# Kernel tuning notes

Measured on AMD Instinct MI355X. Metric: run time of the kernel, lower is better.

Reference implementation:

```python
import jax, jax.numpy as jnp
import numpy as np
from jax import lax

B, N, C, RED = 8, 2048, 1024, 4
GN_EPS = 1e-5


def setup_inputs() -> dict:
    key = jax.random.key(0)
    ks = jax.random.split(key, 8)
    s = lambda k, shp, sc: jax.random.normal(k, shp, jnp.float32) * sc
    return dict(
        x=jax.random.normal(ks[0], (B, N, C), jnp.float32),
        qkv_w=s(ks[1], (C, 3 * C), 0.02),
        c1=jnp.float32(0.01 ** 2),
        c2=jnp.float32(0.03 ** 2),
        conv1_w=s(ks[2], (4, 1, 3), 0.3),      # OIH
        gn_g=jnp.ones(4, jnp.float32),
        gn_b=jnp.zeros(4, jnp.float32),
        conv2_w=s(ks[3], (1, 4, 3), 0.3),      # OIH
        conv2_b=jnp.zeros(1, jnp.float32),
        ch_w1=s(ks[4], (C, C // RED), 0.02),
        ch_b1=jnp.zeros(C // RED, jnp.float32),
        ch_w2=s(ks[5], (C // RED, C), 0.02),
        ch_b2=jnp.zeros(C, jnp.float32),
        proj_w=s(ks[6], (C, C), 0.02),
        proj_b=jnp.zeros(C, jnp.float32),
    )


def _conv1d(x, w):  # x:[B,Cin,N], w:[O,I,3], pad=1
    return lax.conv_general_dilated(x, w, (1,), [(1, 1)],
                                    dimension_numbers=('NCH', 'OIH', 'NCH'))


def _ode_func(A, conv1_w, gn_g, gn_b, conv2_w, conv2_b):
    # A: [B,N] -> Conv1d(1,4) -> GroupNorm(2,4) -> ReLU -> Conv1d(4,1)
    h = _conv1d(A[:, None, :], conv1_w)                 # [B,4,N]
    b, _, n = h.shape
    hg = h.reshape(b, 2, 2, n)                          # 2 groups of 2 channels
    mu = hg.mean((2, 3), keepdims=True)
    var = hg.var((2, 3), keepdims=True)
    h = ((hg - mu) * lax.rsqrt(var + GN_EPS)).reshape(b, 4, n)
    h = jax.nn.relu(h * gn_g[None, :, None] + gn_b[None, :, None])
    y = _conv1d(h, conv2_w) + conv2_b[None, :, None]    # [B,1,N]
    return y[:, 0, :]


def reference(x, qkv_w, c1, c2, conv1_w, gn_g, gn_b, conv2_w, conv2_b,
              ch_w1, ch_b1, ch_w2, ch_b2, proj_w, proj_b):
    Bx, Nx, Cx = x.shape
    qkv = (x @ qkv_w).reshape(Bx, Nx, 3, Cx)
    q, k, v = qkv[..., 0, :], qkv[..., 1, :], qkv[..., 2, :]

    # SSIM-style per-token statistics over the channel dim
    mu_q = q.mean(-1, keepdims=True)
    mu_k = k.mean(-1, keepdims=True)
    dq, dk = q - mu_q, k - mu_k
    inv_cm1 = 1.0 / (Cx - 1)
    sigma_qk = (dq * dk).sum(-1, keepdims=True) * inv_cm1
    sigma_q2 = (dq * dq).sum(-1, keepdims=True) * inv_cm1
    sigma_k2 = (dk * dk).sum(-1, keepdims=True) * inv_cm1
    num = (2 * mu_q * mu_k + c1) * (2 * sigma_qk + c2)
    den = (mu_q ** 2 + mu_k ** 2 + c1) * (sigma_q2 + sigma_k2 + c2)
    attn_base = ((num / (den + 1e-7)) ** 2)[..., 0]     # [B,N]

    # explicit-Euler integration over t = linspace(0,1,2) -> one step, dt=1
    steps = 2
    ts = jnp.linspace(0.0, 1.0, steps)
    dts = ts[1:] - ts[:-1]

    def step(A, dt):
        return A + dt * _ode_func(A, conv1_w, gn_g, gn_b, conv2_w, conv2_b), None

    A, _ = lax.scan(step, attn_base, dts)
    final_a = jax.nn.sigmoid(A)                         # [B,N]
    weights = jax.nn.softmax(final_a, axis=1)           # softmax over tokens

    # channel gating from mean token
    m = x.mean(axis=1, keepdims=True)                   # [B,1,C]
    ch_w = jax.nn.sigmoid(jax.nn.relu(m @ ch_w1 + ch_b1) @ ch_w2 + ch_b2)

    out_low = weights[..., None] * v * ch_w             # [B,N,C]
    return out_low @ proj_w + proj_b
```

## Files before the change

kernel.cpp:

```cpp
#include <hip/hip_runtime.h>

typedef __attribute__((ext_vector_type(8))) short short8;
typedef __attribute__((ext_vector_type(4))) short short4v;
typedef __attribute__((ext_vector_type(4))) float floatx4;

__device__ __forceinline__ unsigned short f2bf(float f) {
    unsigned u = __float_as_uint(f);
    u = u + 0x7fffu + ((u >> 16) & 1u);
    return (unsigned short)(u >> 16);
}

__device__ __forceinline__ void gl_lds16(const void* g, void* l) {
    __builtin_amdgcn_global_load_lds((const __attribute__((address_space(1))) void*)g,
                                     (__attribute__((address_space(3))) void*)l, 16, 0, 0);
}

__global__ __launch_bounds__(256) void convmean_kernel(const float* __restrict__ x,
                                                       short* __restrict__ xb,
                                                       float* __restrict__ part) {
    int bid = blockIdx.x;
    int b = bid >> 6, nch = bid & 63;
    int tid = threadIdx.x;
    size_t base = ((size_t)b * 2048 + nch * 32) * 1024;
    float s0 = 0.f, s1 = 0.f, s2 = 0.f, s3 = 0.f;
    int c0 = tid * 4;
    for (int r = 0; r < 32; r++) {
        const float* rp = x + base + (size_t)r * 1024 + c0;
        float4 v = *(const float4*)rp;
        s0 += v.x; s1 += v.y; s2 += v.z; s3 += v.w;
        short4v o;
        o[0] = (short)f2bf(v.x); o[1] = (short)f2bf(v.y);
        o[2] = (short)f2bf(v.z); o[3] = (short)f2bf(v.w);
        *(short4v*)(xb + base + (size_t)r * 1024 + c0) = o;
    }
    float* pp = part + ((size_t)b * 64 + nch) * 1024 + c0;
    float4 ps; ps.x = s0; ps.y = s1; ps.z = s2; ps.w = s3;
    *(float4*)pp = ps;
}

__global__ __launch_bounds__(256) void transpose_conv_kernel(const float* __restrict__ w_qkv,
                                                             short* __restrict__ qkvT,
                                                             const float* __restrict__ w_proj,
                                                             short* __restrict__ projT) {
    __shared__ float t[64][65];
    int bx = blockIdx.x;
    const float* in; short* out; int C; bool is_qkv;
    int c0, r0 = blockIdx.y * 64;
    if (bx < 48) { in = w_qkv; out = qkvT; C = 3072; c0 = bx * 64; is_qkv = true; }
    else         { in = w_proj; out = projT; C = 1024; c0 = (bx - 48) * 64; is_qkv = false; }
    int tid = threadIdx.x;
#pragma unroll
    for (int l = 0; l < 16; l++) {
        int idx = l * 256 + tid;
        int rr = idx >> 6, cc = idx & 63;
        t[rr][cc] = in[(size_t)(r0 + rr) * C + c0 + cc];
    }
    __syncthreads();
#pragma unroll
    for (int l = 0; l < 16; l++) {
        int idx = l * 256 + tid;
        int rr = idx >> 6, cc = idx & 63;
        int ro = c0 + rr;
        int rnew = ro;
        if (is_qkv) {
            if (ro < 1024) rnew = 2 * ro;
            else if (ro < 2048) rnew = 2 * (ro - 1024) + 1;
        }
        out[(size_t)rnew * 1024 + r0 + cc] = (short)f2bf(t[cc][rr]);
    }
}

__global__ __launch_bounds__(256) void ch_kernel(const float* __restrict__ part,
                                                 const float* __restrict__ w1,
                                                 const float* __restrict__ b1,
                                                 const float* __restrict__ w2,
                                                 const float* __restrict__ b2,
                                                 float* __restrict__ ch) {
    int b = blockIdx.x >> 3, cg = blockIdx.x & 7;
    int tid = threadIdx.x;
    __shared__ float mrow[1024];
    __shared__ float hid[256];
    for (int i = tid; i < 1024; i += 256) {
        float s = 0.f;
        for (int j = 0; j < 64; j++) s += part[((size_t)b * 64 + j) * 1024 + i];
        mrow[i] = s * (1.f / 2048.f);
    }
    __syncthreads();
    {
        float s0 = 0.f, s1 = 0.f, s2 = 0.f, s3 = 0.f;
        for (int i = 0; i < 1024; i += 4) {
            s0 += mrow[i] * w1[(size_t)i * 256 + tid];
            s1 += mrow[i + 1] * w1[(size_t)(i + 1) * 256 + tid];
            s2 += mrow[i + 2] * w1[(size_t)(i + 2) * 256 + tid];
            s3 += mrow[i + 3] * w1[(size_t)(i + 3) * 256 + tid];
        }
        hid[tid] = fmaxf((s0 + s1) + (s2 + s3) + b1[tid], 0.f);
    }
    __syncthreads();
    if (tid < 128) {
        int c = cg * 128 + tid;
        float s0 = 0.f, s1 = 0.f, s2 = 0.f, s3 = 0.f;
        for (int j = 0; j < 256; j += 4) {
            s0 += hid[j] * w2[(size_t)j * 1024 + c];
            s1 += hid[j + 1] * w2[(size_t)(j + 1) * 1024 + c];
            s2 += hid[j + 2] * w2[(size_t)(j + 2) * 1024 + c];
            s3 += hid[j + 3] * w2[(size_t)(j + 3) * 1024 + c];
        }
        float s = (s0 + s1) + (s2 + s3) + b2[c];
        ch[(size_t)b * 1024 + c] = 1.f / (1.f + expf(-s));
    }
}


#define QKV_PHASE(qq)                                                                   \
    {                                                                                   \
        _Pragma("unroll")                                                               \
        for (int ii = 0; ii < 4; ii++)                                                  \
            af[ii] = *(const short8*)(As_ + (wm * 128 + ((qq)*4 + ii) * 16 + ar) * 32 + swq); \
        __builtin_amdgcn_s_setprio(1);                                                  \
        _Pragma("unroll")                                                               \
        for (int ii = 0; ii < 4; ii++)                                                  \
            _Pragma("unroll")                                                           \
            for (int jj = 0; jj < 4; jj++)                                              \
                acc[(qq)*4 + ii][jj] =                                                  \
                    __builtin_amdgcn_mfma_f32_16x16x32_bf16(af[ii], bfr[jj], acc[(qq)*4 + ii][jj], 0, 0, 0); \
        __builtin_amdgcn_s_setprio(0);                                                  \
    }

#define LOAD_B()                                                                        \
    {                                                                                   \
        _Pragma("unroll")                                                               \
        for (int jj = 0; jj < 4; jj++)                                                  \
            bfr[jj] = *(const short8*)(Bs_ + (wn * 64 + jj * 16 + ar) * 32 + swq);      \
    }

__global__ __launch_bounds__(512, 2) void gemm_qkv_kernel(const short* __restrict__ A,
                                                          const short* __restrict__ BT,
                                                          short* __restrict__ vbuf,
                                                          const float* __restrict__ ch,
                                                          float* __restrict__ part2)
{
    __shared__ __align__(16) short ASf[4 * 8192];
    __shared__ __align__(16) short BSf[4 * 8192];
    const int tid = threadIdx.x;
    const int wave = tid >> 6, lane = tid & 63;
    const int id = blockIdx.x;
    const int xcd = id & 7, j = id >> 3;
    const int bn = j % 12;
    const int bmg = j / 12;
    const int bm = bmg * 8 + xcd;
    const int wm = wave >> 2, wn = wave & 3;
    const int ar = lane & 15, quad = lane >> 4;
    const int swq = (quad ^ ((ar >> 1) & 3)) * 8;

    const int swzk = ((lane & 3) ^ ((lane >> 3) & 3)) * 8;
    const short* Ag = A + (size_t)(bm * 256 + wave * 32 + (lane >> 2)) * 1024 + swzk;
    const short* Bg = BT + (size_t)(bn * 256 + wave * 32 + (lane >> 2)) * 1024 + swzk;
    short* ASw = ASf + wave * 1024;
    short* BSw = BSf + wave * 1024;

    floatx4 acc[8][4];
    floatx4 zero = {0.f, 0.f, 0.f, 0.f};
#pragma unroll
    for (int i = 0; i < 8; i++)
#pragma unroll
        for (int jj = 0; jj < 4; jj++) acc[i][jj] = zero;

    auto stageA = [&](int t) {
        const int sl = (t & 3) * 8192, ko = t * 32;
        gl_lds16(Ag + ko, ASw + sl);
        gl_lds16(Ag + (size_t)16 * 1024 + ko, ASw + sl + 512);
    };
    auto stageB = [&](int t) {
        const int sl = (t & 3) * 8192, ko = t * 32;
        gl_lds16(Bg + ko, BSw + sl);
        gl_lds16(Bg + (size_t)16 * 1024 + ko, BSw + sl + 512);
    };

    short8 af[4], bfr[4];

    stageA(0); stageB(0); stageA(1); stageB(1);
    for (int t = 0; t < 30; ++t) {
        stageA(t + 2);
        asm volatile("s_waitcnt vmcnt(6)" ::: "memory");
        asm volatile("s_barrier" ::: "memory");
        const short* As_ = ASf + (t & 3) * 8192;
        const short* Bs_ = BSf + (t & 3) * 8192;
        LOAD_B();
        QKV_PHASE(0);
        stageB(t + 2);
        QKV_PHASE(1);
    }
    {
        asm volatile("s_waitcnt vmcnt(4)" ::: "memory");
        asm volatile("s_barrier" ::: "memory");
        const short* As_ = ASf + (30 & 3) * 8192;
        const short* Bs_ = BSf + (30 & 3) * 8192;
        LOAD_B();
        QKV_PHASE(0);
        QKV_PHASE(1);
    }
    {
        asm volatile("s_waitcnt vmcnt(0)" ::: "memory");
        asm volatile("s_barrier" ::: "memory");
        const short* As_ = ASf + (31 & 3) * 8192;
        const short* Bs_ = BSf + (31 & 3) * 8192;
        LOAD_B();
        QKV_PHASE(0);
        QKV_PHASE(1);
    }
    __syncthreads();

    if (bn < 8) {
        float* sb = (float*)ASf;
#pragma unroll
        for (int i = 0; i < 8; i++) {
            float st[4][5];
#pragma unroll
            for (int r = 0; r < 4; r++)
#pragma unroll
                for (int f = 0; f < 5; f++) st[r][f] = 0.f;
#pragma unroll
            for (int jj = 0; jj < 4; jj++) {
#pragma unroll
                for (int r = 0; r < 4; r++) {
                    float val = acc[i][jj][r];
                    float other = __shfl_xor(val, 1);
                    float q = (lane & 1) ? other : val;
                    float kv = (lane & 1) ? val : other;
                    st[r][0] += q; st[r][1] += kv;
                    st[r][2] += q * q; st[r][3] += kv * kv; st[r][4] += q * kv;
                }
            }
#pragma unroll
            for (int r = 0; r < 4; r++)
#pragma unroll
                for (int f = 0; f < 5; f++) {
                    float v = st[r][f];
                    v += __shfl_xor(v, 2);
                    v += __shfl_xor(v, 4);
                    v += __shfl_xor(v, 8);
                    st[r][f] = v;
                }
            if ((lane & 15) == 0) {
#pragma unroll
                for (int r = 0; r < 4; r++)
#pragma unroll
                    for (int f = 0; f < 5; f++)
                        sb[(size_t)(wn * 256 + wm * 128 + i * 16 + quad * 4 + r) * 5 + f] = st[r][f];
            }
        }
        __syncthreads();
        if (tid < 256) {
#pragma unroll
            for (int f = 0; f < 5; f++) {
                float s = sb[(size_t)(0 * 256 + tid) * 5 + f] + sb[(size_t)(1 * 256 + tid) * 5 + f] +
                          sb[(size_t)(2 * 256 + tid) * 5 + f] + sb[(size_t)(3 * 256 + tid) * 5 + f];
                part2[(size_t)(bn * 5 + f) * 16384 + bm * 256 + tid] = s;
            }
        }
    } else {
        const int batch = bm >> 3;
        const int vcol0 = bn * 256 - 2048 + wn * 64;
        short* pbuf = (short*)ASf + wave * 1024;
        float cw[4];
#pragma unroll
        for (int jj = 0; jj < 4; jj++) cw[jj] = ch[(size_t)batch * 1024 + vcol0 + jj * 16 + ar];
#pragma unroll
        for (int i = 0; i < 8; i++) {
#pragma unroll
            for (int jj = 0; jj < 4; jj++)
#pragma unroll
                for (int r = 0; r < 4; r++)
                    pbuf[(quad * 4 + r) * 64 + jj * 16 + ar] = (short)f2bf(acc[i][jj][r] * cw[jj]);
#pragma unroll
            for (int p = 0; p < 2; p++) {
                int idx = p * 512 + lane * 8;
                short8 vv = *(const short8*)(pbuf + idx);
                int grow = bm * 256 + wm * 128 + i * 16 + (idx >> 6);
                int gcol = vcol0 + (idx & 63);
                *(short8*)(vbuf + (size_t)grow * 1024 + gcol) = vv;
            }
        }
    }
}

__global__ __launch_bounds__(256) void finalize_kernel(const float* __restrict__ part2,
                                                       const float* __restrict__ c1p,
                                                       const float* __restrict__ c2p,
                                                       float* __restrict__ attn) {
    int row = blockIdx.x * 256 + threadIdx.x;
    float s[5] = {0.f, 0.f, 0.f, 0.f, 0.f};
#pragma unroll
    for (int slot = 0; slot < 8; slot++)
#pragma unroll
        for (int f = 0; f < 5; f++)
            s[f] += part2[(size_t)((slot * 5 + f) << 14) + row];
    const float C = 1024.f, invcm1 = 1.f / 1023.f;
    float c1 = *c1p, c2 = *c2p;
    float muq = s[0] / C, muk = s[1] / C;
    float sigqk = (s[4] - C * muq * muk) * invcm1;
    float sigq2 = (s[2] - C * muq * muq) * invcm1;
    float sigk2 = (s[3] - C * muk * muk) * invcm1;
    float num = (2.f * muq * muk + c1) * (2.f * sigqk + c2);
    float den = (muq * muq + muk * muk + c1) * (sigq2 + sigk2 + c2);
    float r = num / (den + 1e-7f);
    attn[row] = r * r;
}

__device__ __forceinline__ float blk_sum(float v, float* buf) {
#pragma unroll
    for (int m = 1; m < 64; m <<= 1) v += __shfl_xor(v, m);
    int wave = threadIdx.x >> 6;
    if ((threadIdx.x & 63) == 0) buf[wave] = v;
    __syncthreads();
    float r = buf[0] + buf[1] + buf[2] + buf[3];
    __syncthreads();
    return r;
}
__device__ __forceinline__ float blk_max(float v, float* buf) {
#pragma unroll
    for (int m = 1; m < 64; m <<= 1) v = fmaxf(v, __shfl_xor(v, m));
    int wave = threadIdx.x >> 6;
    if ((threadIdx.x & 63) == 0) buf[wave] = v;
    __syncthreads();
    float r = fmaxf(fmaxf(buf[0], buf[1]), fmaxf(buf[2], buf[3]));
    __syncthreads();
    return r;
}

__global__ __launch_bounds__(256) void ode_softmax_kernel(const float* __restrict__ attn,
                                                          const float* __restrict__ w1,
                                                          const float* __restrict__ gng,
                                                          const float* __restrict__ gnb,
                                                          const float* __restrict__ w2,
                                                          const float* __restrict__ b2,
                                                          float* __restrict__ wgt) {
    int b = blockIdx.x, tid = threadIdx.x;
    __shared__ float A0[2048];
    __shared__ float H[4][2048];
    __shared__ float rbuf[4];
    for (int i = tid; i < 2048; i += 256) A0[i] = attn[(size_t)b * 2048 + i];
    __syncthreads();
    float w1l[12], w2l[12];
#pragma unroll
    for (int i = 0; i < 12; i++) { w1l[i] = w1[i]; w2l[i] = w2[i]; }
    float gg[4], gb[4];
#pragma unroll
    for (int c = 0; c < 4; c++) { gg[c] = gng[c]; gb[c] = gnb[c]; }

    float s0 = 0.f, ss0 = 0.f, s1 = 0.f, ss1 = 0.f;
    for (int i = tid; i < 2048; i += 256) {
        float le = (i > 0) ? A0[i - 1] : 0.f;
        float mi = A0[i];
        float ri = (i < 2047) ? A0[i + 1] : 0.f;
#pragma unroll
        for (int c = 0; c < 4; c++) {
            float h = w1l[c * 3] * le + w1l[c * 3 + 1] * mi + w1l[c * 3 + 2] * ri;
            H[c][i] = h;
            if (c < 2) { s0 += h; ss0 += h * h; } else { s1 += h; ss1 += h * h; }
        }
    }
    s0 = blk_sum(s0, rbuf);
    ss0 = blk_sum(ss0, rbuf);
    s1 = blk_sum(s1, rbuf);
    ss1 = blk_sum(ss1, rbuf);
    float mu0 = s0 / 4096.f, var0 = ss0 / 4096.f - mu0 * mu0;
    float mu1 = s1 / 4096.f, var1 = ss1 / 4096.f - mu1 * mu1;
    float is0 = 1.f / sqrtf(var0 + 1e-5f);
    float is1 = 1.f / sqrtf(var1 + 1e-5f);

    for (int i = tid; i < 2048; i += 256) {
#pragma unroll
        for (int c = 0; c < 4; c++) {
            float inv = (c < 2) ? is0 : is1;
            float mu = (c < 2) ? mu0 : mu1;
            float v = (H[c][i] - mu) * inv * gg[c] + gb[c];
            H[c][i] = fmaxf(v, 0.f);
        }
    }
    __syncthreads();

    float bias2 = b2[0];
    float myfa[8];
    float lmax = -1e30f;
#pragma unroll
    for (int ii = 0; ii < 8; ii++) {
        int i = tid + ii * 256;
        float y = bias2;
#pragma unroll
        for (int c = 0; c < 4; c++) {
            float le = (i > 0) ? H[c][i - 1] : 0.f;
            float mi = H[c][i];
            float ri = (i < 2047) ? H[c][i + 1] : 0.f;
            y += w2l[c * 3] * le + w2l[c * 3 + 1] * mi + w2l[c * 3 + 2] * ri;
        }
        float Av = A0[i] + y;
        float fa = 1.f / (1.f + expf(-Av));
        myfa[ii] = fa;
        lmax = fmaxf(lmax, fa);
    }
    float gmax = blk_max(lmax, rbuf);
    float lsum = 0.f;
#pragma unroll
    for (int ii = 0; ii < 8; ii++) {
        myfa[ii] = expf(myfa[ii] - gmax);
        lsum += myfa[ii];
    }
    float gsum = blk_sum(lsum, rbuf);
    float inv = 1.f / gsum;
#pragma unroll
    for (int ii = 0; ii < 8; ii++) wgt[(size_t)b * 2048 + tid + ii * 256] = myfa[ii] * inv;
}

__global__ __launch_bounds__(512, 2) void gemm_out_kernel(const short* __restrict__ vbuf,
                                                          const short* __restrict__ BT,
                                                          const float* __restrict__ wgt,
                                                          const float* __restrict__ pb,
                                                          float* __restrict__ Out)
{
    __shared__ __align__(16) short ASf[4 * 8192];
    __shared__ __align__(16) short BSf[4 * 8192];
    const int tid = threadIdx.x;
    const int wave = tid >> 6, lane = tid & 63;
    const int id = blockIdx.x;
    const int xcd = id & 7, j = id >> 3;
    const int bn = j & 3;
    const int bmg = j >> 2;
    const int bm = bmg * 8 + xcd;
    const int wm = wave >> 2, wn = wave & 3;
    const int ar = lane & 15, quad = lane >> 4;
    const int swq = (quad ^ ((ar >> 1) & 3)) * 8;

    const int swzk = ((lane & 3) ^ ((lane >> 3) & 3)) * 8;
    const short* Ag = vbuf + (size_t)(bm * 256 + wave * 32 + (lane >> 2)) * 1024 + swzk;
    const short* Bg = BT + (size_t)(bn * 256 + wave * 32 + (lane >> 2)) * 1024 + swzk;
    short* ASw = ASf + wave * 1024;
    short* BSw = BSf + wave * 1024;

    floatx4 acc[8][4];
    floatx4 zero = {0.f, 0.f, 0.f, 0.f};
#pragma unroll
    for (int i = 0; i < 8; i++)
#pragma unroll
        for (int jj = 0; jj < 4; jj++) acc[i][jj] = zero;

    auto stageA = [&](int t) {
        const int sl = (t & 3) * 8192, ko = t * 32;
        gl_lds16(Ag + ko, ASw + sl);
        gl_lds16(Ag + (size_t)16 * 1024 + ko, ASw + sl + 512);
    };
    auto stageB = [&](int t) {
        const int sl = (t & 3) * 8192, ko = t * 32;
        gl_lds16(Bg + ko, BSw + sl);
        gl_lds16(Bg + (size_t)16 * 1024 + ko, BSw + sl + 512);
    };

    short8 af[4], bfr[4];

    stageA(0); stageB(0); stageA(1); stageB(1);
    for (int t = 0; t < 30; ++t) {
        stageA(t + 2);
        asm volatile("s_waitcnt vmcnt(6)" ::: "memory");
        asm volatile("s_barrier" ::: "memory");
        const short* As_ = ASf + (t & 3) * 8192;
        const short* Bs_ = BSf + (t & 3) * 8192;
        LOAD_B();
        QKV_PHASE(0);
        stageB(t + 2);
        QKV_PHASE(1);
    }
    {
        asm volatile("s_waitcnt vmcnt(4)" ::: "memory");
        asm volatile("s_barrier" ::: "memory");
        const short* As_ = ASf + (30 & 3) * 8192;
        const short* Bs_ = BSf + (30 & 3) * 8192;
        LOAD_B();
        QKV_PHASE(0);
        QKV_PHASE(1);
    }
    {
        asm volatile("s_waitcnt vmcnt(0)" ::: "memory");
        asm volatile("s_barrier" ::: "memory");
        const short* As_ = ASf + (31 & 3) * 8192;
        const short* Bs_ = BSf + (31 & 3) * 8192;
        LOAD_B();
        QKV_PHASE(0);
        QKV_PHASE(1);
    }
    __syncthreads();

    const int row0 = bm * 256 + wm * 128;
    const int col0 = bn * 256 + wn * 64;
    float* obuf = (float*)ASf + wave * 1024;
#pragma unroll
    for (int i = 0; i < 8; i++) {
#pragma unroll
        for (int jj = 0; jj < 4; jj++) {
            float bias = pb[col0 + jj * 16 + ar];
#pragma unroll
            for (int r = 0; r < 4; r++) {
                int grow = row0 + i * 16 + quad * 4 + r;
                obuf[(quad * 4 + r) * 64 + jj * 16 + ar] = wgt[grow] * acc[i][jj][r] + bias;
            }
        }
#pragma unroll
        for (int p = 0; p < 4; p++) {
            int idx = p * 256 + lane * 4;
            float4 vv = *(const float4*)(obuf + idx);
            int grow = row0 + i * 16 + (idx >> 6);
            int gcol = col0 + (idx & 63);
            *(float4*)(Out + (size_t)grow * 1024 + gcol) = vv;
        }
    }
}

extern "C" void kernel_launch(void* const* d_in, const int* in_sizes, int n_in,
                              void* d_out, int out_size, void* d_ws, size_t ws_size,
                              hipStream_t stream) {
    const float* x       = (const float*)d_in[0];
    const float* qkv_w   = (const float*)d_in[1];
    const float* c1      = (const float*)d_in[2];
    const float* c2      = (const float*)d_in[3];
    const float* conv1_w = (const float*)d_in[4];
    const float* gn_g    = (const float*)d_in[5];
    const float* gn_b    = (const float*)d_in[6];
    const float* conv2_w = (const float*)d_in[7];
    const float* conv2_b = (const float*)d_in[8];
    const float* ch_w1   = (const float*)d_in[9];
    const float* ch_b1   = (const float*)d_in[10];
    const float* ch_w2   = (const float*)d_in[11];
    const float* ch_b2   = (const float*)d_in[12];
    const float* proj_w  = (const float*)d_in[13];
    const float* proj_b  = (const float*)d_in[14];
    float* out = (float*)d_out;

    size_t off = 0;
    char* base = (char*)d_ws;
    auto carve = [&](size_t bytes) -> char* {
        char* p = base + off;
        off += (bytes + 255) & ~(size_t)255;
        return p;
    };
    short* x_bf  = (short*)carve((size_t)16384 * 1024 * 2);
    short* qkvT  = (short*)carve((size_t)3072 * 1024 * 2);
    short* projT = (short*)carve((size_t)1024 * 1024 * 2);
    short* vbuf  = (short*)carve((size_t)16384 * 1024 * 2);
    float* part2 = (float*)carve((size_t)80 * 16384 * 4);
    float* attn  = (float*)carve((size_t)16384 * 4);
    float* wgt   = (float*)carve((size_t)16384 * 4);
    float* part  = (float*)carve((size_t)8 * 64 * 1024 * 4);
    float* chw   = (float*)carve((size_t)8 * 1024 * 4);

    convmean_kernel<<<512, 256, 0, stream>>>(x, x_bf, part);
    transpose_conv_kernel<<<dim3(64, 16), 256, 0, stream>>>(qkv_w, qkvT, proj_w, projT);
    ch_kernel<<<64, 256, 0, stream>>>(part, ch_w1, ch_b1, ch_w2, ch_b2, chw);
    gemm_qkv_kernel<<<768, 512, 0, stream>>>(x_bf, qkvT, vbuf, chw, part2);
    finalize_kernel<<<64, 256, 0, stream>>>(part2, c1, c2, attn);
    ode_softmax_kernel<<<8, 256, 0, stream>>>(attn, conv1_w, gn_g, gn_b, conv2_w, conv2_b, wgt);
    gemm_out_kernel<<<256, 512, 0, stream>>>(vbuf, projT, wgt, proj_b, out);
}
```

Baseline: 390.9 us.

## Restructure GEMM main loop into ping-pong LDS-fragment and MFMA phases with extra barriers

Both bf16 GEMM kernels now load LDS fragments into two separate A-fragment register sets and issue global-to-LDS staging between the fragment reads and the MFMA blocks. Barriers are placed inside each half-iteration, and the vmcnt wait moves to the end of the iteration. The aim is to overlap LDS reads and global prefetch with MFMA work and keep waves in lockstep in a ping-pong style schedule. The cost is more barriers per iteration and more register pressure from the second A-fragment array, which could hurt occupancy at launch bounds 512,2.

```diff
diff --git a/kernel.cpp b/kernel.cpp
--- a/kernel.cpp
+++ b/kernel.cpp
@@ -112,26 +112,30 @@
 }
 
 
-#define QKV_PHASE(qq)                                                                   \
+#define LOAD_BF()                                                                       \
+    {                                                                                   \
+        _Pragma("unroll")                                                               \
+        for (int jj = 0; jj < 4; jj++)                                                  \
+            bfr[jj] = *(const short8*)(Bs_ + (wn * 64 + jj * 16 + ar) * 32 + swq);      \
+    }
+
+#define LOAD_AF(dst, qq)                                                                \
     {                                                                                   \
         _Pragma("unroll")                                                               \
         for (int ii = 0; ii < 4; ii++)                                                  \
-            af[ii] = *(const short8*)(As_ + (wm * 128 + ((qq)*4 + ii) * 16 + ar) * 32 + swq); \
+            dst[ii] = *(const short8*)(As_ + (wm * 128 + ((qq)*4 + ii) * 16 + ar) * 32 + swq); \
+    }
+
+#define MFMA_Q(afv, qq)                                                                 \
+    {                                                                                   \
         __builtin_amdgcn_s_setprio(1);                                                  \
         _Pragma("unroll")                                                               \
         for (int ii = 0; ii < 4; ii++)                                                  \
             _Pragma("unroll")                                                           \
             for (int jj = 0; jj < 4; jj++)                                              \
                 acc[(qq)*4 + ii][jj] =                                                  \
-                    __builtin_amdgcn_mfma_f32_16x16x32_bf16(af[ii], bfr[jj], acc[(qq)*4 + ii][jj], 0, 0, 0); \
+                    __builtin_amdgcn_mfma_f32_16x16x32_bf16(afv[ii], bfr[jj], acc[(qq)*4 + ii][jj], 0, 0, 0); \
         __builtin_amdgcn_s_setprio(0);                                                  \
-    }
-
-#define LOAD_B()                                                                        \
-    {                                                                                   \
-        _Pragma("unroll")                                                               \
-        for (int jj = 0; jj < 4; jj++)                                                  \
-            bfr[jj] = *(const short8*)(Bs_ + (wn * 64 + jj * 16 + ar) * 32 + swq);      \
     }
 
 __global__ __launch_bounds__(512, 2) void gemm_qkv_kernel(const short* __restrict__ A,
@@ -177,37 +181,40 @@
         gl_lds16(Bg + (size_t)16 * 1024 + ko, BSw + sl + 512);
     };
 
-    short8 af[4], bfr[4];
+    short8 af0[4], af1[4], bfr[4];
 
     stageA(0); stageB(0); stageA(1); stageB(1);
+    asm volatile("s_waitcnt vmcnt(4)" ::: "memory");
+    asm volatile("s_barrier" ::: "memory");
     for (int t = 0; t < 30; ++t) {
-        stageA(t + 2);
-        asm volatile("s_waitcnt vmcnt(6)" ::: "memory");
-        asm volatile("s_barrier" ::: "memory");
         const short* As_ = ASf + (t & 3) * 8192;
         const short* Bs_ = BSf + (t & 3) * 8192;
-        LOAD_B();
-        QKV_PHASE(0);
+        LOAD_BF();
+        LOAD_AF(af0, 0);
+        stageA(t + 2);
+        asm volatile("s_barrier" ::: "memory");
+        MFMA_Q(af0, 0);
+        LOAD_AF(af1, 1);
         stageB(t + 2);
-        QKV_PHASE(1);
-    }
-    {
+        asm volatile("s_barrier" ::: "memory");
+        MFMA_Q(af1, 1);
         asm volatile("s_waitcnt vmcnt(4)" ::: "memory");
         asm volatile("s_barrier" ::: "memory");
-        const short* As_ = ASf + (30 & 3) * 8192;
-        const short* Bs_ = BSf + (30 & 3) * 8192;
-        LOAD_B();
-        QKV_PHASE(0);
-        QKV_PHASE(1);
-    }
-    {
-        asm volatile("s_waitcnt vmcnt(0)" ::: "memory");
-        asm volatile("s_barrier" ::: "memory");
-        const short* As_ = ASf + (31 & 3) * 8192;
-        const short* Bs_ = BSf + (31 & 3) * 8192;
-        LOAD_B();
-        QKV_PHASE(0);
-        QKV_PHASE(1);
+    }
+    for (int t = 30; t < 32; ++t) {
+        const short* As_ = ASf + (t & 3) * 8192;
+        const short* Bs_ = BSf + (t & 3) * 8192;
+        LOAD_BF();
+        LOAD_AF(af0, 0);
+        asm volatile("s_barrier" ::: "memory");
+        MFMA_Q(af0, 0);
+        LOAD_AF(af1, 1);
+        asm volatile("s_barrier" ::: "memory");
+        MFMA_Q(af1, 1);
+        if (t == 30) {
+            asm volatile("s_waitcnt vmcnt(0)" ::: "memory");
+            asm volatile("s_barrier" ::: "memory");
+        }
     }
     __syncthreads();
 
@@ -456,37 +463,40 @@
         gl_lds16(Bg + (size_t)16 * 1024 + ko, BSw + sl + 512);
     };
 
-    short8 af[4], bfr[4];
+    short8 af0[4], af1[4], bfr[4];
 
     stageA(0); stageB(0); stageA(1); stageB(1);
+    asm volatile("s_waitcnt vmcnt(4)" ::: "memory");
+    asm volatile("s_barrier" ::: "memory");
     for (int t = 0; t < 30; ++t) {
-        stageA(t + 2);
-        asm volatile("s_waitcnt vmcnt(6)" ::: "memory");
-        asm volatile("s_barrier" ::: "memory");
         const short* As_ = ASf + (t & 3) * 8192;
         const short* Bs_ = BSf + (t & 3) * 8192;
-        LOAD_B();
-        QKV_PHASE(0);
+        LOAD_BF();
+        LOAD_AF(af0, 0);
+        stageA(t + 2);
+        asm volatile("s_barrier" ::: "memory");
+        MFMA_Q(af0, 0);
+        LOAD_AF(af1, 1);
         stageB(t + 2);
-        QKV_PHASE(1);
-    }
-    {
+        asm volatile("s_barrier" ::: "memory");
+        MFMA_Q(af1, 1);
         asm volatile("s_waitcnt vmcnt(4)" ::: "memory");
         asm volatile("s_barrier" ::: "memory");
-        const short* As_ = ASf + (30 & 3) * 8192;
-        const short* Bs_ = BSf + (30 & 3) * 8192;
-        LOAD_B();
-        QKV_PHASE(0);
-        QKV_PHASE(1);
-    }
-    {
-        asm volatile("s_waitcnt vmcnt(0)" ::: "memory");
-        asm volatile("s_barrier" ::: "memory");
-        const short* As_ = ASf + (31 & 3) * 8192;
-        const short* Bs_ = BSf + (31 & 3) * 8192;
-        LOAD_B();
-        QKV_PHASE(0);
-        QKV_PHASE(1);
+    }
+    for (int t = 30; t < 32; ++t) {
+        const short* As_ = ASf + (t & 3) * 8192;
+        const short* Bs_ = BSf + (t & 3) * 8192;
+        LOAD_BF();
+        LOAD_AF(af0, 0);
+        asm volatile("s_barrier" ::: "memory");
+        MFMA_Q(af0, 0);
+        LOAD_AF(af1, 1);
+        asm volatile("s_barrier" ::: "memory");
+        MFMA_Q(af1, 1);
+        if (t == 30) {
+            asm volatile("s_waitcnt vmcnt(0)" ::: "memory");
+            asm volatile("s_barrier" ::: "memory");
+        }
     }
     __syncthreads();
 
```

Result: slower. 399.7 us (+2.3%).

## Interleave GEMM main loop into four barrier-separated phases with split staging loads

Applied to the files above, without the earlier changes.

Restructures the K-loop of both bf16 GEMM kernels so each tile is processed in four phases of two A-fragment rows, each issuing one global-to-LDS load and then a workgroup barrier before its MFMAs. The aim is to spread memory issue evenly across the MFMA stream and keep the waves in lockstep, ping-pong style, so LDS reads and global loads overlap compute better. It adds several extra barriers per tile, which can cost throughput if the waves drift apart. It also moves the waitcnt to the end of each tile.

```diff
diff --git a/kernel.cpp b/kernel.cpp
--- a/kernel.cpp
+++ b/kernel.cpp
@@ -112,26 +112,44 @@
 }
 
 
-#define QKV_PHASE(qq)                                                                   \
-    {                                                                                   \
-        _Pragma("unroll")                                                               \
-        for (int ii = 0; ii < 4; ii++)                                                  \
-            af[ii] = *(const short8*)(As_ + (wm * 128 + ((qq)*4 + ii) * 16 + ar) * 32 + swq); \
-        __builtin_amdgcn_s_setprio(1);                                                  \
-        _Pragma("unroll")                                                               \
-        for (int ii = 0; ii < 4; ii++)                                                  \
-            _Pragma("unroll")                                                           \
-            for (int jj = 0; jj < 4; jj++)                                              \
-                acc[(qq)*4 + ii][jj] =                                                  \
-                    __builtin_amdgcn_mfma_f32_16x16x32_bf16(af[ii], bfr[jj], acc[(qq)*4 + ii][jj], 0, 0, 0); \
-        __builtin_amdgcn_s_setprio(0);                                                  \
-    }
-
-#define LOAD_B()                                                                        \
+#define LDB4()                                                                          \
     {                                                                                   \
         _Pragma("unroll")                                                               \
         for (int jj = 0; jj < 4; jj++)                                                  \
             bfr[jj] = *(const short8*)(Bs_ + (wn * 64 + jj * 16 + ar) * 32 + swq);      \
+    }
+
+#define PH(qq, STAGE)                                                                   \
+    {                                                                                   \
+        short8 a0 = *(const short8*)(As_ + (wm * 128 + ((qq)*2 + 0) * 16 + ar) * 32 + swq); \
+        short8 a1 = *(const short8*)(As_ + (wm * 128 + ((qq)*2 + 1) * 16 + ar) * 32 + swq); \
+        STAGE;                                                                          \
+        asm volatile("s_barrier" ::: "memory");                                         \
+        __builtin_amdgcn_sched_barrier(0);                                              \
+        __builtin_amdgcn_s_setprio(1);                                                  \
+        _Pragma("unroll")                                                               \
+        for (int jj = 0; jj < 4; jj++)                                                  \
+            acc[(qq)*2 + 0][jj] =                                                       \
+                __builtin_amdgcn_mfma_f32_16x16x32_bf16(a0, bfr[jj], acc[(qq)*2 + 0][jj], 0, 0, 0); \
+        _Pragma("unroll")                                                               \
+        for (int jj = 0; jj < 4; jj++)                                                  \
+            acc[(qq)*2 + 1][jj] =                                                       \
+                __builtin_amdgcn_mfma_f32_16x16x32_bf16(a1, bfr[jj], acc[(qq)*2 + 1][jj], 0, 0, 0); \
+        __builtin_amdgcn_s_setprio(0);                                                  \
+    }
+
+#define TILE_BODY(T, SA0, SA1, SB0, SB1)                                                \
+    {                                                                                   \
+        const short* As_ = ASf + ((T) & 3) * 8192;                                      \
+        const short* Bs_ = BSf + ((T) & 3) * 8192;                                      \
+        LDB4();                                                                         \
+        PH(0, SA0);                                                                     \
+        asm volatile("s_barrier" ::: "memory");                                         \
+        PH(1, SA1);                                                                     \
+        asm volatile("s_barrier" ::: "memory");                                         \
+        PH(2, SB0);                                                                     \
+        asm volatile("s_barrier" ::: "memory");                                         \
+        PH(3, SB1);                                                                     \
     }
 
 __global__ __launch_bounds__(512, 2) void gemm_qkv_kernel(const short* __restrict__ A,
@@ -166,49 +184,26 @@
 #pragma unroll
         for (int jj = 0; jj < 4; jj++) acc[i][jj] = zero;
 
-    auto stageA = [&](int t) {
-        const int sl = (t & 3) * 8192, ko = t * 32;
-        gl_lds16(Ag + ko, ASw + sl);
-        gl_lds16(Ag + (size_t)16 * 1024 + ko, ASw + sl + 512);
-    };
-    auto stageB = [&](int t) {
-        const int sl = (t & 3) * 8192, ko = t * 32;
-        gl_lds16(Bg + ko, BSw + sl);
-        gl_lds16(Bg + (size_t)16 * 1024 + ko, BSw + sl + 512);
-    };
-
-    short8 af[4], bfr[4];
-
-    stageA(0); stageB(0); stageA(1); stageB(1);
+    auto stA0 = [&](int t) { gl_lds16(Ag + t * 32, ASw + (t & 3) * 8192); };
+    auto stA1 = [&](int t) { gl_lds16(Ag + (size_t)16 * 1024 + t * 32, ASw + (t & 3) * 8192 + 512); };
+    auto stB0 = [&](int t) { gl_lds16(Bg + t * 32, BSw + (t & 3) * 8192); };
+    auto stB1 = [&](int t) { gl_lds16(Bg + (size_t)16 * 1024 + t * 32, BSw + (t & 3) * 8192 + 512); };
+
+    short8 bfr[4];
+
+    stA0(0); stA1(0); stB0(0); stB1(0);
+    stA0(1); stA1(1); stB0(1); stB1(1);
+    asm volatile("s_waitcnt vmcnt(4)" ::: "memory");
+    asm volatile("s_barrier" ::: "memory");
     for (int t = 0; t < 30; ++t) {
-        stageA(t + 2);
-        asm volatile("s_waitcnt vmcnt(6)" ::: "memory");
-        asm volatile("s_barrier" ::: "memory");
-        const short* As_ = ASf + (t & 3) * 8192;
-        const short* Bs_ = BSf + (t & 3) * 8192;
-        LOAD_B();
-        QKV_PHASE(0);
-        stageB(t + 2);
-        QKV_PHASE(1);
-    }
-    {
+        TILE_BODY(t, stA0(t + 2), stA1(t + 2), stB0(t + 2), stB1(t + 2));
         asm volatile("s_waitcnt vmcnt(4)" ::: "memory");
         asm volatile("s_barrier" ::: "memory");
-        const short* As_ = ASf + (30 & 3) * 8192;
-        const short* Bs_ = BSf + (30 & 3) * 8192;
-        LOAD_B();
-        QKV_PHASE(0);
-        QKV_PHASE(1);
-    }
-    {
-        asm volatile("s_waitcnt vmcnt(0)" ::: "memory");
-        asm volatile("s_barrier" ::: "memory");
-        const short* As_ = ASf + (31 & 3) * 8192;
-        const short* Bs_ = BSf + (31 & 3) * 8192;
-        LOAD_B();
-        QKV_PHASE(0);
-        QKV_PHASE(1);
-    }
+    }
+    TILE_BODY(30, , , , );
+    asm volatile("s_waitcnt vmcnt(0)" ::: "memory");
+    asm volatile("s_barrier" ::: "memory");
+    TILE_BODY(31, , , , );
     __syncthreads();
 
     if (bn < 8) {
@@ -445,49 +440,26 @@
 #pragma unroll
         for (int jj = 0; jj < 4; jj++) acc[i][jj] = zero;
 
-    auto stageA = [&](int t) {
-        const int sl = (t & 3) * 8192, ko = t * 32;
-        gl_lds16(Ag + ko, ASw + sl);
-        gl_lds16(Ag + (size_t)16 * 1024 + ko, ASw + sl + 512);
-    };
-    auto stageB = [&](int t) {
-        const int sl = (t & 3) * 8192, ko = t * 32;
-        gl_lds16(Bg + ko, BSw + sl);
-        gl_lds16(Bg + (size_t)16 * 1024 + ko, BSw + sl + 512);
-    };
-
-    short8 af[4], bfr[4];
-
-    stageA(0); stageB(0); stageA(1); stageB(1);
+    auto stA0 = [&](int t) { gl_lds16(Ag + t * 32, ASw + (t & 3) * 8192); };
+    auto stA1 = [&](int t) { gl_lds16(Ag + (size_t)16 * 1024 + t * 32, ASw + (t & 3) * 8192 + 512); };
+    auto stB0 = [&](int t) { gl_lds16(Bg + t * 32, BSw + (t & 3) * 8192); };
+    auto stB1 = [&](int t) { gl_lds16(Bg + (size_t)16 * 1024 + t * 32, BSw + (t & 3) * 8192 + 512); };
+
+    short8 bfr[4];
+
+    stA0(0); stA1(0); stB0(0); stB1(0);
+    stA0(1); stA1(1); stB0(1); stB1(1);
+    asm volatile("s_waitcnt vmcnt(4)" ::: "memory");
+    asm volatile("s_barrier" ::: "memory");
     for (int t = 0; t < 30; ++t) {
-        stageA(t + 2);
-        asm volatile("s_waitcnt vmcnt(6)" ::: "memory");
-        asm volatile("s_barrier" ::: "memory");
-        const short* As_ = ASf + (t & 3) * 8192;
-        const short* Bs_ = BSf + (t & 3) * 8192;
-        LOAD_B();
-        QKV_PHASE(0);
-        stageB(t + 2);
-        QKV_PHASE(1);
-    }
-    {
+        TILE_BODY(t, stA0(t + 2), stA1(t + 2), stB0(t + 2), stB1(t + 2));
         asm volatile("s_waitcnt vmcnt(4)" ::: "memory");
         asm volatile("s_barrier" ::: "memory");
-        const short* As_ = ASf + (30 & 3) * 8192;
-        const short* Bs_ = BSf + (30 & 3) * 8192;
-        LOAD_B();
-        QKV_PHASE(0);
-        QKV_PHASE(1);
-    }
-    {
-        asm volatile("s_waitcnt vmcnt(0)" ::: "memory");
-        asm volatile("s_barrier" ::: "memory");
-        const short* As_ = ASf + (31 & 3) * 8192;
-        const short* Bs_ = BSf + (31 & 3) * 8192;
-        LOAD_B();
-        QKV_PHASE(0);
-        QKV_PHASE(1);
-    }
+    }
+    TILE_BODY(30, , , , );
+    asm volatile("s_waitcnt vmcnt(0)" ::: "memory");
+    asm volatile("s_barrier" ::: "memory");
+    TILE_BODY(31, , , , );
     __syncthreads();
 
     const int row0 = bm * 256 + wm * 128;
```

Result: slower. 406.3 us (+3.9%).
